# Performance work log

Hardware: AMD Instinct MI355X
Metric: run time of the kernel (lower is better)

The kernel has to match this reference:

```python
import jax, jax.numpy as jnp
import numpy as np

N_NODES = 50000
N_EDGES = 800000
D_MODEL = 128
N_HEADS = 2
N_LAYERS = 2
NEG_SLOPE = 0.2


def setup_inputs() -> dict:
    key = jax.random.key(0)
    ks = jax.random.split(key, 7)
    x = jax.random.normal(ks[0], (N_NODES, D_MODEL), dtype=jnp.float32)
    Ws = jax.random.normal(ks[1], (N_LAYERS, D_MODEL, N_HEADS * D_MODEL), dtype=jnp.float32) * (1.0 / np.sqrt(D_MODEL))
    als = jax.random.normal(ks[2], (N_LAYERS, N_HEADS, D_MODEL), dtype=jnp.float32) * (1.0 / np.sqrt(D_MODEL))
    ars = jax.random.normal(ks[3], (N_LAYERS, N_HEADS, D_MODEL), dtype=jnp.float32) * (1.0 / np.sqrt(D_MODEL))
    bs = jax.random.normal(ks[4], (N_LAYERS, N_HEADS, D_MODEL), dtype=jnp.float32) * 0.01
    src = jax.random.randint(ks[5], (N_EDGES,), 0, N_NODES, dtype=jnp.int32)
    dst = jax.random.randint(ks[6], (N_EDGES,), 0, N_NODES, dtype=jnp.int32)
    return {"x": x, "Ws": Ws, "als": als, "ars": ars, "bs": bs, "src": src, "dst": dst}


def _gat_layer(h, W, al, ar, b, src, dst, n_nodes):
    # h: (N, D); W: (D, H*F); al/ar/b: (H, F)
    H, F = al.shape
    feat = (h @ W).reshape(n_nodes, H, F)                      # (N, H, F)
    el = jnp.einsum('nhf,hf->nh', feat, al)                    # (N, H)
    er = jnp.einsum('nhf,hf->nh', feat, ar)                    # (N, H)
    e = jax.nn.leaky_relu(el[src] + er[dst], NEG_SLOPE)        # (E, H)
    # edge softmax over incoming edges of each dst node, per head
    emax = jax.lax.stop_gradient(jax.ops.segment_max(e, dst, num_segments=n_nodes))
    ex = jnp.exp(e - emax[dst])
    denom = jax.ops.segment_sum(ex, dst, num_segments=n_nodes)  # (N, H)
    alpha = ex / denom[dst]                                     # (E, H)
    msg = feat[src] * alpha[:, :, None]                         # (E, H, F)
    out = jax.ops.segment_sum(msg, dst, num_segments=n_nodes) + b  # (N, H, F)
    return out


def reference(x, Ws, als, ars, bs, src, dst):
    n_nodes = x.shape[0]
    h = x
    out = None
    for i in range(N_LAYERS):
        out = _gat_layer(h, Ws[i], als[i], ars[i], bs[i], src, dst, n_nodes)
        h = out.mean(axis=1)  # merge heads to feed next layer
    return out  # (N, H, F)
```

## Files before the change

kernel.cpp:

```cpp
#include <hip/hip_runtime.h>
#include <hip/hip_bf16.h>


#define NEG_SLOPE 0.2f
#define SEG_CAP 160

typedef __attribute__((ext_vector_type(8))) short bf16x8_t;
typedef __attribute__((ext_vector_type(4))) float f32x4_t;

__device__ __forceinline__ unsigned short f2bf(float f) {
  union { float f; unsigned int u; } v; v.f = f;
  unsigned int r = v.u + 0x7FFFu + ((v.u >> 16) & 1u);
  return (unsigned short)(r >> 16);
}
__device__ __forceinline__ float bfbits(unsigned int hi16) {
  union { unsigned int u; float f; } v; v.u = hi16;
  return v.f;
}


__global__ __launch_bounds__(256) void init_kernel(
    const float* __restrict__ Ws, const float* __restrict__ als,
    const float* __restrict__ ars,
    unsigned short* __restrict__ Whi, unsigned short* __restrict__ Wlo,
    float* __restrict__ wal, float* __restrict__ war,
    int* __restrict__ bcur2, unsigned int* __restrict__ tstate,
    int n, int nb32)
{
  const int b = blockIdx.x;
  const int t = threadIdx.x;
  if (b < 32) {
    int tg = b * 256 + t;
    int t2 = tg & 4095;
    int lane = t2 & 63;
    int ct3 = (t2 >> 6) & 7;
    int s = (t2 >> 9) & 3;
    int hb = (t2 >> 11) & 1;
    int lay = tg >> 12;
    int col = hb * 128 + ct3 * 16 + (lane & 15);
    int kbase = s * 32 + (lane >> 4) * 8;
    size_t obase = (size_t)lay * 32768 + (size_t)hb * 16384 + (size_t)(t2 & 2047) * 8;
    #pragma unroll
    for (int j = 0; j < 8; ++j) {
      float w = Ws[(size_t)lay * 32768 + (size_t)(kbase + j) * 256 + col];
      unsigned short hb16 = f2bf(w);
      float rem = w - bfbits((unsigned int)hb16 << 16);
      Whi[obase + j] = hb16;
      Wlo[obase + j] = f2bf(rem);
    }
  } else if (b < 36) {
    int tg = (b - 32) * 256 + t;
    int lr = tg >> 9;
    int rem = tg & 511;
    int lay = rem >> 8, h = (rem >> 7) & 1, k = rem & 127;
    const float* a = (lr ? ars : als) + (size_t)lay * 256 + h * 128;
    const float* wrow = Ws + (size_t)lay * 32768 + (size_t)k * 256 + h * 128;
    float sum = 0.f;
    for (int f = 0; f < 128; ++f) sum = fmaf(wrow[f], a[f], sum);
    (lr ? war : wal)[(size_t)lay * 256 + h * 128 + k] = sum;
  } else {
    int idx = (b - 36) * 256 + t;
    if (idx < nb32 * 8) {
      int c = idx / nb32;
      int bb = idx - c * nb32;
      bcur2[idx] = (bb * 8 + c) * SEG_CAP;
    }
    if (idx < 512) tstate[idx] = 0u;
  }
}


__global__ __launch_bounds__(256) void binAx_kernel(
    const int* __restrict__ src, const int* __restrict__ dst,
    int* __restrict__ bcur2, unsigned int* __restrict__ tmp,
    int nb32, int n_edges, int histBlocks,
    const float* __restrict__ x, const float* __restrict__ wal,
    const float* __restrict__ war, unsigned short* __restrict__ xb16,
    float* __restrict__ el, float* __restrict__ er, int n)
{
  const int b = blockIdx.x;
  if (b < histBlocks) {
    int e = b * 256 + threadIdx.x;
    if (e < n_edges) {
      int d = dst[e];
      int p = atomicAdd(&bcur2[(b & 7) * nb32 + (d >> 5)], 1);
      tmp[p] = ((unsigned int)(d & 127) << 16) | (unsigned int)src[e];
    }
    return;
  }
  int node = (b - histBlocks) * 4 + (threadIdx.x >> 6);
  int c = threadIdx.x & 63;
  if (node >= n) return;
  float2 v = *(const float2*)&x[(size_t)node * 128 + c * 2];
  unsigned int pk = (unsigned int)f2bf(v.x) | ((unsigned int)f2bf(v.y) << 16);
  *(unsigned int*)&xb16[(size_t)node * 128 + c * 2] = pk;
  float pl0 = v.x * wal[2 * c] + v.y * wal[2 * c + 1];
  float pl1 = v.x * wal[128 + 2 * c] + v.y * wal[128 + 2 * c + 1];
  float pr0 = v.x * war[2 * c] + v.y * war[2 * c + 1];
  float pr1 = v.x * war[128 + 2 * c] + v.y * war[128 + 2 * c + 1];
  #pragma unroll
  for (int off = 1; off < 64; off <<= 1) {
    pl0 += __shfl_xor(pl0, off);
    pl1 += __shfl_xor(pl1, off);
    pr0 += __shfl_xor(pr0, off);
    pr1 += __shfl_xor(pr1, off);
  }
  if (c == 0) {
    *(float2*)&el[(size_t)node * 2] = make_float2(pl0, pl1);
    *(float2*)&er[(size_t)node * 2] = make_float2(pr0, pr1);
  }
}


__global__ __launch_bounds__(256) void binB_kernel(
    const unsigned int* __restrict__ tmp, const int* __restrict__ bcur2,
    int* __restrict__ offsets, int* __restrict__ srcp,
    unsigned int* __restrict__ tstate, int nb32, int n_nodes, int nregions)
{
  __shared__ int cnt[128];
  __shared__ int cur[128];
  __shared__ int w0tot;
  __shared__ int s_total;
  __shared__ int s_pfx;
  const int b = blockIdx.x;
  const int t = threadIdx.x;
  const int base = b * 128;
  int bb0 = b * 4;
  int bb1 = bb0 + 4; if (bb1 > nb32) bb1 = nb32;

  if (t < 128) cnt[t] = 0;
  __syncthreads();
  for (int bb = bb0; bb < bb1; ++bb) {
    #pragma unroll
    for (int c8 = 0; c8 < 8; ++c8) {
      int segbase = (bb * 8 + c8) * SEG_CAP;
      int fill = bcur2[c8 * nb32 + bb] - segbase;
      for (int j = t; j < fill; j += 256) {
        atomicAdd(&cnt[tmp[segbase + j] >> 16], 1);
      }
    }
  }
  __syncthreads();
  int v = 0, inc = 0;
  if (t < 128) {
    v = cnt[t];
    inc = v;
    #pragma unroll
    for (int off = 1; off < 64; off <<= 1) {
      int u = __shfl_up(inc, off);
      if ((t & 63) >= off) inc += u;
    }
    if (t == 63) w0tot = inc;
    cnt[t] = inc - v;
  }
  __syncthreads();
  if (t == 127) s_total = cnt[127] + w0tot + v;
  __syncthreads();
  if (t == 0) {
    int total = s_total;
    atomicExch(&tstate[b], 0x40000000u | (unsigned)total);
    int prefix = 0;
    int i = b - 1;
    while (i >= 0) {
      unsigned st = atomicAdd(&tstate[i], 0u);
      unsigned fl = st >> 30;
      if (fl == 0u) continue;
      prefix += (int)(st & 0x3FFFFFFFu);
      if (fl == 2u) break;
      --i;
    }
    atomicExch(&tstate[b], 0x80000000u | (unsigned)(prefix + total));
    s_pfx = prefix;
    if (b == nregions - 1) offsets[n_nodes] = prefix + total;
  }
  __syncthreads();
  if (t < 128) {
    int ex = cnt[t] + ((t >= 64) ? w0tot : 0);
    int node = base + t;
    int off = s_pfx + ex;
    if (node < n_nodes) offsets[node] = off;
    cur[t] = off;
  }
  __syncthreads();
  for (int bb = bb0; bb < bb1; ++bb) {
    #pragma unroll
    for (int c8 = 0; c8 < 8; ++c8) {
      int segbase = (bb * 8 + c8) * SEG_CAP;
      int fill = bcur2[c8 * nb32 + bb] - segbase;
      for (int j = t; j < fill; j += 256) {
        unsigned int q = tmp[segbase + j];
        int p = atomicAdd(&cur[q >> 16], 1);
        srcp[p] = (int)(q & 0xFFFFu);
      }
    }
  }
}


#define AGG_E(qj, xj)                                               \
  {                                                                 \
    float f0 = bfbits(qj << 16), f1 = bfbits(qj & 0xFFFF0000u);     \
    a00 = fmaf(xj.x, f0, a00); a01 = fmaf(xj.x, f1, a01);           \
    a10 = fmaf(xj.y, f0, a10); a11 = fmaf(xj.y, f1, a11);           \
  }

__global__ __launch_bounds__(256) void aggregate_kernel(
    const unsigned short* __restrict__ hsrc,
    const float* __restrict__ el, const float* __restrict__ er,
    const int* __restrict__ srcp, const int* __restrict__ offsets,
    unsigned int* __restrict__ agghi, int n_nodes)
{
  __shared__ int s_s[4][64];
  __shared__ float2 s_x[4][64];
  const int wid = threadIdx.x >> 6;
  const int c = threadIdx.x & 63;
  int node = blockIdx.x * 4 + wid;
  if (node >= n_nodes) return;
  int beg = offsets[node];
  int end = offsets[node + 1];
  float2 ern = *(const float2*)&er[(size_t)node * 2];

  float a00 = 0.f, a01 = 0.f, a10 = 0.f, a11 = 0.f;
  float den0 = 0.f, den1 = 0.f;

  for (int chunk = beg; chunk < end; chunk += 64) {
    int m = end - chunk; if (m > 64) m = 64;
    if (c < m) {
      int s = srcp[chunk + c];
      float2 l = *(const float2*)&el[(size_t)s * 2];
      float e0 = l.x + ern.x;
      float e1 = l.y + ern.y;
      e0 = fminf((e0 >= 0.f) ? e0 : NEG_SLOPE * e0, 60.f);
      e1 = fminf((e1 >= 0.f) ? e1 : NEG_SLOPE * e1, 60.f);
      float x0 = __expf(e0), x1 = __expf(e1);
      den0 += x0; den1 += x1;
      s_s[wid][c] = s;
      s_x[wid][c] = make_float2(x0, x1);
    }
    __builtin_amdgcn_wave_barrier();
    int e = 0;
    for (; e + 8 <= m; e += 8) {
      int s0 = s_s[wid][e + 0], s1 = s_s[wid][e + 1], s2 = s_s[wid][e + 2], s3 = s_s[wid][e + 3];
      int s4 = s_s[wid][e + 4], s5 = s_s[wid][e + 5], s6 = s_s[wid][e + 6], s7 = s_s[wid][e + 7];
      float2 x0 = s_x[wid][e + 0], x1 = s_x[wid][e + 1], x2 = s_x[wid][e + 2], x3 = s_x[wid][e + 3];
      float2 x4 = s_x[wid][e + 4], x5 = s_x[wid][e + 5], x6 = s_x[wid][e + 6], x7 = s_x[wid][e + 7];
      unsigned int q0 = *(const unsigned int*)&hsrc[(size_t)s0 * 128 + c * 2];
      unsigned int q1 = *(const unsigned int*)&hsrc[(size_t)s1 * 128 + c * 2];
      unsigned int q2 = *(const unsigned int*)&hsrc[(size_t)s2 * 128 + c * 2];
      unsigned int q3 = *(const unsigned int*)&hsrc[(size_t)s3 * 128 + c * 2];
      unsigned int q4 = *(const unsigned int*)&hsrc[(size_t)s4 * 128 + c * 2];
      unsigned int q5 = *(const unsigned int*)&hsrc[(size_t)s5 * 128 + c * 2];
      unsigned int q6 = *(const unsigned int*)&hsrc[(size_t)s6 * 128 + c * 2];
      unsigned int q7 = *(const unsigned int*)&hsrc[(size_t)s7 * 128 + c * 2];
      AGG_E(q0, x0)
      AGG_E(q1, x1)
      AGG_E(q2, x2)
      AGG_E(q3, x3)
      AGG_E(q4, x4)
      AGG_E(q5, x5)
      AGG_E(q6, x6)
      AGG_E(q7, x7)
    }
    for (; e < m; ++e) {
      int s0 = s_s[wid][e];
      float2 x0 = s_x[wid][e];
      unsigned int q0 = *(const unsigned int*)&hsrc[(size_t)s0 * 128 + c * 2];
      AGG_E(q0, x0)
    }
    __builtin_amdgcn_wave_barrier();
  }

  #pragma unroll
  for (int off = 32; off > 0; off >>= 1) {
    den0 += __shfl_xor(den0, off);
    den1 += __shfl_xor(den1, off);
  }

  float o00 = 0.f, o01 = 0.f, o10 = 0.f, o11 = 0.f;
  if (end > beg) {
    float i0 = 1.0f / den0, i1 = 1.0f / den1;
    o00 = a00 * i0; o01 = a01 * i0;
    o10 = a10 * i1; o11 = a11 * i1;
  }
  unsigned int hi0 = (unsigned int)f2bf(o00) | ((unsigned int)f2bf(o01) << 16);
  unsigned int hi1 = (unsigned int)f2bf(o10) | ((unsigned int)f2bf(o11) << 16);
  agghi[(size_t)node * 128 + c]      = hi0;
  agghi[(size_t)node * 128 + 64 + c] = hi1;
}


__global__ __launch_bounds__(256) void gemm1_kernel(
    const unsigned short* __restrict__ agghi,
    const unsigned short* __restrict__ Whi, const unsigned short* __restrict__ Wlo,
    const float* __restrict__ wal2, const float* __restrict__ war2,
    const float* __restrict__ b0,
    unsigned short* __restrict__ hb16, float* __restrict__ el, float* __restrict__ er,
    int n_nodes)
{
  __shared__ unsigned short lds_bh[16384];
  __shared__ unsigned short lds_bl[16384];
  const int tid = threadIdx.x;
  const int w = tid >> 6;
  const int lane = tid & 63;
  const int lrow = lane & 15;
  const int g = lane >> 4;
  const int node0 = blockIdx.x * 64 + w * 16;

  int arow = node0 + lrow;
  int arow_c = (arow < n_nodes) ? arow : (n_nodes - 1);

  f32x4_t acc[8];
  #pragma unroll
  for (int i = 0; i < 8; ++i) acc[i] = (f32x4_t){0.f, 0.f, 0.f, 0.f};

  for (int hb = 0; hb < 2; ++hb) {
    __syncthreads();
    {
      const uint4* gh = (const uint4*)(Whi + (size_t)hb * 16384);
      const uint4* gl = (const uint4*)(Wlo + (size_t)hb * 16384);
      uint4* lh = (uint4*)lds_bh;
      uint4* ll = (uint4*)lds_bl;
      #pragma unroll
      for (int r = 0; r < 8; ++r) {
        lh[tid + 256 * r] = gh[tid + 256 * r];
        ll[tid + 256 * r] = gl[tid + 256 * r];
      }
    }
    __syncthreads();
    const unsigned short* ah_p = agghi + (size_t)arow_c * 256 + hb * 128 + g * 8;
    #pragma unroll
    for (int s = 0; s < 4; ++s) {
      bf16x8_t ahi = *(const bf16x8_t*)(ah_p + s * 32);
      #pragma unroll
      for (int ct = 0; ct < 8; ++ct) {
        bf16x8_t bh = *(const bf16x8_t*)&lds_bh[((s * 8 + ct) * 64 + lane) * 8];
        bf16x8_t bl = *(const bf16x8_t*)&lds_bl[((s * 8 + ct) * 64 + lane) * 8];
        acc[ct] = __builtin_amdgcn_mfma_f32_16x16x32_bf16(ahi, bh, acc[ct], 0, 0, 0);
        acc[ct] = __builtin_amdgcn_mfma_f32_16x16x32_bf16(ahi, bl, acc[ct], 0, 0, 0);
      }
    }
  }

  float bm[8], alc0[8], alc1[8], arc0[8], arc1[8];
  #pragma unroll
  for (int ct = 0; ct < 8; ++ct) {
    int col = ct * 16 + lrow;
    bm[ct] = 0.5f * (b0[col] + b0[128 + col]);
    alc0[ct] = wal2[col];
    alc1[ct] = wal2[128 + col];
    arc0[ct] = war2[col];
    arc1[ct] = war2[128 + col];
  }
  #pragma unroll
  for (int r = 0; r < 4; ++r) {
    int orow = node0 + g * 4 + r;
    bool ok = orow < n_nodes;
    float pl0 = 0.f, pl1 = 0.f, pr0 = 0.f, pr1 = 0.f;
    #pragma unroll
    for (int ct = 0; ct < 8; ++ct) {
      float v = fmaf(acc[ct][r], 0.5f, bm[ct]);
      pl0 += v * alc0[ct];
      pl1 += v * alc1[ct];
      pr0 += v * arc0[ct];
      pr1 += v * arc1[ct];
      if (ok) hb16[(size_t)orow * 128 + ct * 16 + lrow] = f2bf(v);
    }
    #pragma unroll
    for (int off = 1; off < 16; off <<= 1) {
      pl0 += __shfl_xor(pl0, off);
      pl1 += __shfl_xor(pl1, off);
      pr0 += __shfl_xor(pr0, off);
      pr1 += __shfl_xor(pr1, off);
    }
    if (lrow == 0 && ok) {
      *(float2*)&el[(size_t)orow * 2] = make_float2(pl0, pl1);
      *(float2*)&er[(size_t)orow * 2] = make_float2(pr0, pr1);
    }
  }
}


__global__ __launch_bounds__(256) void gemm2_kernel(
    const unsigned short* __restrict__ agghi,
    const unsigned short* __restrict__ Whi, const unsigned short* __restrict__ Wlo,
    const float* __restrict__ b1, float* __restrict__ out, int n_nodes)
{
  __shared__ unsigned short lds_bh[16384];
  __shared__ unsigned short lds_bl[16384];
  const int tid = threadIdx.x;
  const int w = tid >> 6;
  const int lane = tid & 63;
  const int lrow = lane & 15;
  const int g = lane >> 4;
  const int hb = blockIdx.y;
  const int node0 = blockIdx.x * 64 + w * 16;

  {
    const uint4* gh = (const uint4*)(Whi + (size_t)hb * 16384);
    const uint4* gl = (const uint4*)(Wlo + (size_t)hb * 16384);
    uint4* lh = (uint4*)lds_bh;
    uint4* ll = (uint4*)lds_bl;
    #pragma unroll
    for (int r = 0; r < 8; ++r) {
      lh[tid + 256 * r] = gh[tid + 256 * r];
      ll[tid + 256 * r] = gl[tid + 256 * r];
    }
  }

  int arow = node0 + lrow;
  int arow_c = (arow < n_nodes) ? arow : (n_nodes - 1);
  const unsigned short* ah_p = agghi + (size_t)arow_c * 256 + hb * 128 + g * 8;

  f32x4_t acc[8];
  #pragma unroll
  for (int i = 0; i < 8; ++i) acc[i] = (f32x4_t){0.f, 0.f, 0.f, 0.f};

  __syncthreads();

  #pragma unroll
  for (int s = 0; s < 4; ++s) {
    bf16x8_t ahi = *(const bf16x8_t*)(ah_p + s * 32);
    #pragma unroll
    for (int ct = 0; ct < 8; ++ct) {
      bf16x8_t bh = *(const bf16x8_t*)&lds_bh[((s * 8 + ct) * 64 + lane) * 8];
      bf16x8_t bl = *(const bf16x8_t*)&lds_bl[((s * 8 + ct) * 64 + lane) * 8];
      acc[ct] = __builtin_amdgcn_mfma_f32_16x16x32_bf16(ahi, bh, acc[ct], 0, 0, 0);
      acc[ct] = __builtin_amdgcn_mfma_f32_16x16x32_bf16(ahi, bl, acc[ct], 0, 0, 0);
    }
  }

  float bc[8];
  #pragma unroll
  for (int ct = 0; ct < 8; ++ct) bc[ct] = b1[hb * 128 + ct * 16 + lrow];
  #pragma unroll
  for (int r = 0; r < 4; ++r) {
    int orow = node0 + g * 4 + r;
    if (orow >= n_nodes) continue;
    #pragma unroll
    for (int ct = 0; ct < 8; ++ct) {
      out[(size_t)orow * 256 + hb * 128 + ct * 16 + lrow] = acc[ct][r] + bc[ct];
    }
  }
}


extern "C" void kernel_launch(void* const* d_in, const int* in_sizes, int n_in,
                              void* d_out, int out_size, void* d_ws, size_t ws_size,
                              hipStream_t stream) {
  const float* x   = (const float*)d_in[0];
  const float* Ws  = (const float*)d_in[1];
  const float* als = (const float*)d_in[2];
  const float* ars = (const float*)d_in[3];
  const float* bs  = (const float*)d_in[4];
  const int*   src = (const int*)d_in[5];
  const int*   dst = (const int*)d_in[6];
  const int N = in_sizes[0] / 128;
  const int E = in_sizes[5];
  float* out = (float*)d_out;

  char* ws = (char*)d_ws;
  auto alloc = [&](size_t bytes) {
    char* p = ws;
    ws += (bytes + 255) & ~(size_t)255;
    return p;
  };
  const int nb32 = (N + 31) / 32;

  unsigned int* agghi = (unsigned int*)alloc((size_t)N * 128 * 4);
  unsigned short* xb16 = (unsigned short*)alloc((size_t)N * 128 * 2);
  unsigned short* hb16 = (unsigned short*)alloc((size_t)N * 128 * 2);
  int*   srcp    = (int*)alloc((size_t)E * 4);
  unsigned int* tmp = (unsigned int*)alloc((size_t)nb32 * 8 * SEG_CAP * 4);
  int*   offsets = (int*)alloc((size_t)(N + 1) * 4);
  int*   bcur2   = (int*)alloc((size_t)nb32 * 8 * 4);
  unsigned int* tstate = (unsigned int*)alloc((size_t)512 * 4);
  float* el      = (float*)alloc((size_t)N * 2 * 4);
  float* er      = (float*)alloc((size_t)N * 2 * 4);
  float* wal     = (float*)alloc((size_t)512 * 4);
  float* war     = (float*)alloc((size_t)512 * 4);
  unsigned short* Whi = (unsigned short*)alloc((size_t)65536 * 2);
  unsigned short* Wlo = (unsigned short*)alloc((size_t)65536 * 2);

  const int init_blocks = 36 + (nb32 * 8 + 255) / 256;
  const int ngrp = (N + 3) / 4;
  const int ntiles = (N + 63) / 64;
  const int nregions = (N + 127) / 128;
  const int histBlocks = (E + 255) / 256;

  init_kernel<<<dim3(init_blocks), dim3(256), 0, stream>>>(
      Ws, als, ars, Whi, Wlo, wal, war, bcur2, tstate, N, nb32);
  binAx_kernel<<<dim3(histBlocks + ngrp), dim3(256), 0, stream>>>(
      src, dst, bcur2, tmp, nb32, E, histBlocks, x, wal, war, xb16, el, er, N);
  binB_kernel<<<dim3(nregions), dim3(256), 0, stream>>>(
      tmp, bcur2, offsets, srcp, tstate, nb32, N, nregions);

  aggregate_kernel<<<dim3(ngrp), dim3(256), 0, stream>>>(
      xb16, el, er, srcp, offsets, agghi, N);
  gemm1_kernel<<<dim3(ntiles), dim3(256), 0, stream>>>(
      (const unsigned short*)agghi, Whi, Wlo, wal + 256, war + 256, bs, hb16, el, er, N);
  aggregate_kernel<<<dim3(ngrp), dim3(256), 0, stream>>>(
      hb16, el, er, srcp, offsets, agghi, N);
  gemm2_kernel<<<dim3(ntiles, 2), dim3(256), 0, stream>>>(
      (const unsigned short*)agghi, Whi + 32768, Wlo + 32768, bs + 256, out, N);
}
```

Before: 204.5 us.

## Pre-bin edges per block in shared memory before global atomic reservation

The edge binning pass now has each block load 4096 edges into LDS and count them per 128-node region. It reserves space with one global atomic per region per class, then scatters the edges into contiguous runs. This replaces one global atomic per edge with far fewer, and makes binB read one segment set per region instead of four 32-node buckets. The cost is larger segment capacity (512 per region-class), a bigger LDS footprint in binAx, and a risk of overflow if a region-class segment exceeds 512 edges.

```diff
diff --git a/kernel.cpp b/kernel.cpp
--- a/kernel.cpp
+++ b/kernel.cpp
@@ -3,7 +3,8 @@
 
 
 #define NEG_SLOPE 0.2f
-#define SEG_CAP 160
+#define SEG_CAP 512
+#define EPB 4096
 
 typedef __attribute__((ext_vector_type(8))) short bf16x8_t;
 typedef __attribute__((ext_vector_type(4))) float f32x4_t;
@@ -24,8 +25,8 @@
     const float* __restrict__ ars,
     unsigned short* __restrict__ Whi, unsigned short* __restrict__ Wlo,
     float* __restrict__ wal, float* __restrict__ war,
-    int* __restrict__ bcur2, unsigned int* __restrict__ tstate,
-    int n, int nb32)
+    int* __restrict__ gcur, unsigned int* __restrict__ tstate,
+    int nregions)
 {
   const int b = blockIdx.x;
   const int t = threadIdx.x;
@@ -60,11 +61,7 @@
     (lr ? war : wal)[(size_t)lay * 256 + h * 128 + k] = sum;
   } else {
     int idx = (b - 36) * 256 + t;
-    if (idx < nb32 * 8) {
-      int c = idx / nb32;
-      int bb = idx - c * nb32;
-      bcur2[idx] = (bb * 8 + c) * SEG_CAP;
-    }
+    if (idx < nregions * 8) gcur[idx] = idx * SEG_CAP;
     if (idx < 512) tstate[idx] = 0u;
   }
 }
@@ -72,24 +69,49 @@
 
 __global__ __launch_bounds__(256) void binAx_kernel(
     const int* __restrict__ src, const int* __restrict__ dst,
-    int* __restrict__ bcur2, unsigned int* __restrict__ tmp,
-    int nb32, int n_edges, int histBlocks,
+    int* __restrict__ gcur, unsigned int* __restrict__ tmp,
+    int n_edges, int binABlocks,
     const float* __restrict__ x, const float* __restrict__ wal,
     const float* __restrict__ war, unsigned short* __restrict__ xb16,
     float* __restrict__ el, float* __restrict__ er, int n)
 {
+  __shared__ unsigned int ebuf[EPB];
+  __shared__ int rcnt[392];
+  __shared__ int rbase[392];
   const int b = blockIdx.x;
-  if (b < histBlocks) {
-    int e = b * 256 + threadIdx.x;
-    if (e < n_edges) {
-      int d = dst[e];
-      int p = atomicAdd(&bcur2[(b & 7) * nb32 + (d >> 5)], 1);
-      tmp[p] = ((unsigned int)(d & 127) << 16) | (unsigned int)src[e];
+  const int t = threadIdx.x;
+  if (b < binABlocks) {
+    const int cls = b & 7;
+    const int base = b * EPB;
+    int nE = n_edges - base; if (nE > EPB) nE = EPB;
+    for (int i = t; i < 392; i += 256) rcnt[i] = 0;
+    __syncthreads();
+    for (int i = t; i < nE; i += 256) {
+      int d = dst[base + i];
+      int s = src[base + i];
+      ebuf[i] = ((unsigned int)d << 16) | (unsigned int)s;
+      atomicAdd(&rcnt[d >> 7], 1);
+    }
+    __syncthreads();
+    for (int r = t; r < 391; r += 256) {
+      int cnt = rcnt[r];
+      int gb = 0;
+      if (cnt > 0) gb = atomicAdd(&gcur[r * 8 + cls], cnt);
+      rbase[r] = gb;
+      rcnt[r] = 0;
+    }
+    __syncthreads();
+    for (int i = t; i < nE; i += 256) {
+      unsigned int q = ebuf[i];
+      int d = (int)(q >> 16);
+      int r = d >> 7;
+      int rank = atomicAdd(&rcnt[r], 1);
+      tmp[rbase[r] + rank] = ((unsigned int)(d & 127) << 16) | (q & 0xFFFFu);
     }
     return;
   }
-  int node = (b - histBlocks) * 4 + (threadIdx.x >> 6);
-  int c = threadIdx.x & 63;
+  int node = (b - binABlocks) * 4 + (t >> 6);
+  int c = t & 63;
   if (node >= n) return;
   float2 v = *(const float2*)&x[(size_t)node * 128 + c * 2];
   unsigned int pk = (unsigned int)f2bf(v.x) | ((unsigned int)f2bf(v.y) << 16);
@@ -113,9 +135,9 @@
 
 
 __global__ __launch_bounds__(256) void binB_kernel(
-    const unsigned int* __restrict__ tmp, const int* __restrict__ bcur2,
+    const unsigned int* __restrict__ tmp, const int* __restrict__ gcur,
     int* __restrict__ offsets, int* __restrict__ srcp,
-    unsigned int* __restrict__ tstate, int nb32, int n_nodes, int nregions)
+    unsigned int* __restrict__ tstate, int n_nodes, int nregions)
 {
   __shared__ int cnt[128];
   __shared__ int cur[128];
@@ -125,19 +147,15 @@
   const int b = blockIdx.x;
   const int t = threadIdx.x;
   const int base = b * 128;
-  int bb0 = b * 4;
-  int bb1 = bb0 + 4; if (bb1 > nb32) bb1 = nb32;
 
   if (t < 128) cnt[t] = 0;
   __syncthreads();
-  for (int bb = bb0; bb < bb1; ++bb) {
-    #pragma unroll
-    for (int c8 = 0; c8 < 8; ++c8) {
-      int segbase = (bb * 8 + c8) * SEG_CAP;
-      int fill = bcur2[c8 * nb32 + bb] - segbase;
-      for (int j = t; j < fill; j += 256) {
-        atomicAdd(&cnt[tmp[segbase + j] >> 16], 1);
-      }
+  #pragma unroll
+  for (int c8 = 0; c8 < 8; ++c8) {
+    int segbase = (b * 8 + c8) * SEG_CAP;
+    int fill = gcur[b * 8 + c8] - segbase;
+    for (int j = t; j < fill; j += 256) {
+      atomicAdd(&cnt[tmp[segbase + j] >> 16], 1);
     }
   }
   __syncthreads();
@@ -182,16 +200,14 @@
     cur[t] = off;
   }
   __syncthreads();
-  for (int bb = bb0; bb < bb1; ++bb) {
-    #pragma unroll
-    for (int c8 = 0; c8 < 8; ++c8) {
-      int segbase = (bb * 8 + c8) * SEG_CAP;
-      int fill = bcur2[c8 * nb32 + bb] - segbase;
-      for (int j = t; j < fill; j += 256) {
-        unsigned int q = tmp[segbase + j];
-        int p = atomicAdd(&cur[q >> 16], 1);
-        srcp[p] = (int)(q & 0xFFFFu);
-      }
+  #pragma unroll
+  for (int c8 = 0; c8 < 8; ++c8) {
+    int segbase = (b * 8 + c8) * SEG_CAP;
+    int fill = gcur[b * 8 + c8] - segbase;
+    for (int j = t; j < fill; j += 256) {
+      unsigned int q = tmp[segbase + j];
+      int p = atomicAdd(&cur[q >> 16], 1);
+      srcp[p] = (int)(q & 0xFFFFu);
     }
   }
 }
@@ -464,15 +480,15 @@
     ws += (bytes + 255) & ~(size_t)255;
     return p;
   };
-  const int nb32 = (N + 31) / 32;
+  const int nregions = (N + 127) / 128;
 
   unsigned int* agghi = (unsigned int*)alloc((size_t)N * 128 * 4);
   unsigned short* xb16 = (unsigned short*)alloc((size_t)N * 128 * 2);
   unsigned short* hb16 = (unsigned short*)alloc((size_t)N * 128 * 2);
   int*   srcp    = (int*)alloc((size_t)E * 4);
-  unsigned int* tmp = (unsigned int*)alloc((size_t)nb32 * 8 * SEG_CAP * 4);
+  unsigned int* tmp = (unsigned int*)alloc((size_t)nregions * 8 * SEG_CAP * 4);
   int*   offsets = (int*)alloc((size_t)(N + 1) * 4);
-  int*   bcur2   = (int*)alloc((size_t)nb32 * 8 * 4);
+  int*   gcur    = (int*)alloc((size_t)nregions * 8 * 4);
   unsigned int* tstate = (unsigned int*)alloc((size_t)512 * 4);
   float* el      = (float*)alloc((size_t)N * 2 * 4);
   float* er      = (float*)alloc((size_t)N * 2 * 4);
@@ -481,18 +497,17 @@
   unsigned short* Whi = (unsigned short*)alloc((size_t)65536 * 2);
   unsigned short* Wlo = (unsigned short*)alloc((size_t)65536 * 2);
 
-  const int init_blocks = 36 + (nb32 * 8 + 255) / 256;
+  const int init_blocks = 36 + (nregions * 8 + 255) / 256;
   const int ngrp = (N + 3) / 4;
   const int ntiles = (N + 63) / 64;
-  const int nregions = (N + 127) / 128;
-  const int histBlocks = (E + 255) / 256;
+  const int binABlocks = (E + EPB - 1) / EPB;
 
   init_kernel<<<dim3(init_blocks), dim3(256), 0, stream>>>(
-      Ws, als, ars, Whi, Wlo, wal, war, bcur2, tstate, N, nb32);
-  binAx_kernel<<<dim3(histBlocks + ngrp), dim3(256), 0, stream>>>(
-      src, dst, bcur2, tmp, nb32, E, histBlocks, x, wal, war, xb16, el, er, N);
+      Ws, als, ars, Whi, Wlo, wal, war, gcur, tstate, nregions);
+  binAx_kernel<<<dim3(binABlocks + ngrp), dim3(256), 0, stream>>>(
+      src, dst, gcur, tmp, E, binABlocks, x, wal, war, xb16, el, er, N);
   binB_kernel<<<dim3(nregions), dim3(256), 0, stream>>>(
-      tmp, bcur2, offsets, srcp, tstate, nb32, N, nregions);
+      tmp, gcur, offsets, srcp, tstate, N, nregions);
 
   aggregate_kernel<<<dim3(ngrp), dim3(256), 0, stream>>>(
       xb16, el, er, srcp, offsets, agghi, N);
```

Measured after the change: 170.8 us. 1.2x faster.
